# Performance work log

Measured on AMD Instinct MI355X. Metric: run time of the kernel, lower is better.

The kernel has to match this reference:

```python
import jax, jax.numpy as jnp
import numpy as np

B, S, D, DOUT, E = 2, 2048, 1024, 1024, 8
DH = 4 * D  # expert hidden size


def setup_inputs() -> dict:
    key = jax.random.key(0)
    ks = jax.random.split(key, 7)
    sc = lambda *sh: 1.0 / np.sqrt(sh[-2]) if len(sh) >= 2 else 0.02
    return {
        "x": jax.random.normal(ks[0], (B, S, D), jnp.float32),
        "Wg": jax.random.normal(ks[1], (D, E), jnp.float32) / np.sqrt(D),
        "bg": jnp.zeros((E,), jnp.float32),
        "W1": jax.random.normal(ks[2], (E, D, DH), jnp.float32) / np.sqrt(D),
        "b1": jax.random.normal(ks[3], (E, DH), jnp.float32) * 0.02,
        "W2": jax.random.normal(ks[4], (E, DH, DOUT), jnp.float32) / np.sqrt(DH),
        "b2": jax.random.normal(ks[5], (E, DOUT), jnp.float32) * 0.02,
    }


def reference(x, Wg, bg, W1, b1, W2, b2):
    # x: [B, S, D] -> flatten tokens (chunking over seq in the original is
    # math-neutral: routing and expert MLP are per-token).
    Bb, Ss, Dd = x.shape
    xt = x.reshape(-1, Dd)                       # [T, D]
    # Gate: softmax then argmax (top-1 routing, output NOT scaled by gate prob)
    gates = jax.nn.softmax(xt @ Wg + bg, axis=-1)  # [T, E]
    sel = jnp.argmax(gates, axis=-1)               # [T]
    nE = W1.shape[0]
    out = jnp.zeros((xt.shape[0], W2.shape[-1]), x.dtype)
    # Grouped expert MLP expressed as masked dense loop over the small fixed
    # expert count (jit-friendly; a fused gather-grouped-GEMM-scatter kernel
    # is the optimization target).
    for e in range(nE):
        h = jax.nn.gelu(xt @ W1[e] + b1[e], approximate=False)  # [T, 4D]
        ye = h @ W2[e] + b2[e]                                  # [T, DOUT]
        out = jnp.where((sel == e)[:, None], ye, out)
    return out.reshape(Bb, Ss, -1)
```

## Files before the change

kernel.cpp:

```cpp
#include <hip/hip_runtime.h>
#include <hip/hip_bf16.h>
#include <math.h>

#define T_TOK 4096
#define DIM   1024
#define NEXP  8
#define DHID  4096
#define NDOUT 1024
#define BM    128
#define MAXTILES 40

typedef short bf16x8 __attribute__((ext_vector_type(8)));
typedef float f32x4 __attribute__((ext_vector_type(4)));

__device__ __forceinline__ unsigned short f2bf(float f) {
  unsigned u = __float_as_uint(f);
  u += 0x7fffu + ((u >> 16) & 1u);
  return (unsigned short)(u >> 16);
}
__device__ __forceinline__ unsigned pack2bf(float a, float b) {
  return (unsigned)f2bf(a) | ((unsigned)f2bf(b) << 16);
}
__device__ __forceinline__ void gl_lds16(const void* g, void* l) {
  __builtin_amdgcn_global_load_lds(
      (const __attribute__((address_space(1))) void*)g,
      (__attribute__((address_space(3))) void*)l, 16, 0, 0);
}

__global__ __launch_bounds__(256)
void gate_kernel(const float* __restrict__ x, const float* __restrict__ Wg,
                 const float* __restrict__ bg, int* __restrict__ sel) {
  int lane = threadIdx.x & 63;
  int wid  = threadIdx.x >> 6;
  int t = blockIdx.x * 4 + wid;
  if (t >= T_TOK) return;
  const float* xr = x + (size_t)t * DIM;
  double acc[NEXP];
#pragma unroll
  for (int e = 0; e < NEXP; e++) acc[e] = 0.0;
  for (int j = 0; j < DIM / 64; j++) {
    int d = lane + j * 64;
    float xv = xr[d];
    const float4* wr = reinterpret_cast<const float4*>(Wg + (size_t)d * NEXP);
    float4 w0 = wr[0], w1 = wr[1];
    acc[0] += (double)xv * (double)w0.x;
    acc[1] += (double)xv * (double)w0.y;
    acc[2] += (double)xv * (double)w0.z;
    acc[3] += (double)xv * (double)w0.w;
    acc[4] += (double)xv * (double)w1.x;
    acc[5] += (double)xv * (double)w1.y;
    acc[6] += (double)xv * (double)w1.z;
    acc[7] += (double)xv * (double)w1.w;
  }
#pragma unroll
  for (int off = 32; off >= 1; off >>= 1) {
#pragma unroll
    for (int e = 0; e < NEXP; e++) acc[e] += __shfl_down(acc[e], off);
  }
  if (lane == 0) {
    double best = acc[0] + (double)bg[0];
    int bi = 0;
#pragma unroll
    for (int e = 1; e < NEXP; e++) {
      double v = acc[e] + (double)bg[e];
      if (v > best) { best = v; bi = e; }
    }
    sel[t] = bi;
  }
}

__global__ void zero_kernel(int* __restrict__ counts) {
  if (threadIdx.x < NEXP) counts[threadIdx.x] = 0;
}

__global__ void hist_kernel(const int* __restrict__ sel, int* __restrict__ counts) {
  __shared__ int lc[NEXP];
  if (threadIdx.x < NEXP) lc[threadIdx.x] = 0;
  __syncthreads();
  int t = blockIdx.x * 256 + threadIdx.x;
  atomicAdd(&lc[sel[t]], 1);
  __syncthreads();
  if (threadIdx.x < NEXP) atomicAdd(&counts[threadIdx.x], lc[threadIdx.x]);
}

__global__ void plan_kernel(const int* __restrict__ counts, int* __restrict__ base,
                            int* __restrict__ cursor, int* __restrict__ tileExpert,
                            int* __restrict__ tilePos, int* __restrict__ tileRows,
                            int* __restrict__ ntiles) {
  if (threadIdx.x == 0) {
    int acc = 0, nt = 0;
    for (int e = 0; e < NEXP; e++) {
      base[e] = acc; cursor[e] = acc;
      int c = counts[e];
      for (int j = 0; j < c; j += BM) {
        tileExpert[nt] = e;
        tilePos[nt]    = acc + j;
        int rem = c - j;
        tileRows[nt]   = rem < BM ? rem : BM;
        nt++;
      }
      acc += c;
    }
    *ntiles = nt;
  }
}

__global__ void scatter_kernel(const int* __restrict__ sel, int* __restrict__ cursor,
                               int* __restrict__ list) {
  __shared__ int lcnt[NEXP];
  __shared__ int lbase[NEXP];
  int tid = threadIdx.x;
  if (tid < NEXP) lcnt[tid] = 0;
  __syncthreads();
  int t = blockIdx.x * 256 + tid;
  int e = sel[t];
  int lpos = atomicAdd(&lcnt[e], 1);
  __syncthreads();
  if (tid < NEXP) lbase[tid] = atomicAdd(&cursor[tid], lcnt[tid]);
  __syncthreads();
  list[lbase[e] + lpos] = t;
}

__global__ __launch_bounds__(256)
void convert_x_kernel(const float* __restrict__ x, unsigned short* __restrict__ xbf) {
  int i = (blockIdx.x * 256 + threadIdx.x) * 8;
  float4 a = *(const float4*)(x + i);
  float4 b = *(const float4*)(x + i + 4);
  uint4 o;
  o.x = pack2bf(a.x, a.y); o.y = pack2bf(a.z, a.w);
  o.z = pack2bf(b.x, b.y); o.w = pack2bf(b.z, b.w);
  *(uint4*)(xbf + i) = o;
}

__global__ __launch_bounds__(256)
void transpose_convert_kernel(const float* __restrict__ in, unsigned short* __restrict__ out,
                              int K, int N) {
  int nb = blockIdx.x, kb = blockIdx.y, e = blockIdx.z;
  const float* inp = in + (size_t)e * K * N;
  unsigned short* outp = out + (size_t)e * N * K;
  __shared__ unsigned short lds[64][72];
  int tx = threadIdx.x;
  int kloc = tx >> 4;
  int n4   = (tx & 15) << 2;
#pragma unroll
  for (int p = 0; p < 4; p++) {
    int k = p * 16 + kloc;
    float4 v = *(const float4*)(inp + (size_t)(kb * 64 + k) * N + nb * 64 + n4);
    lds[n4 + 0][k] = f2bf(v.x);
    lds[n4 + 1][k] = f2bf(v.y);
    lds[n4 + 2][k] = f2bf(v.z);
    lds[n4 + 3][k] = f2bf(v.w);
  }
  __syncthreads();
  int n  = tx >> 2;
  int kq = (tx & 3) << 4;
  uint4 a = *(const uint4*)&lds[n][kq];
  uint4 b = *(const uint4*)&lds[n][kq + 8];
  unsigned short* o = outp + (size_t)(nb * 64 + n) * K + kb * 64 + kq;
  *(uint4*)o = a;
  *(uint4*)(o + 8) = b;
}


__global__ __launch_bounds__(256)
void gemm1_kernel(const unsigned short* __restrict__ xbf, const unsigned short* __restrict__ W1T,
                  const float* __restrict__ b1, const int* __restrict__ list,
                  const int* __restrict__ tileExpert, const int* __restrict__ tilePos,
                  const int* __restrict__ tileRows, const int* __restrict__ ntiles,
                  unsigned short* __restrict__ Hc) {
  int tIdx = blockIdx.y;
  if (tIdx >= *ntiles) return;
  int e = tileExpert[tIdx], posBase = tilePos[tIdx], rows = tileRows[tIdx];
  int n0 = blockIdx.x * 128;

  __shared__ __align__(1024) char As[128 * 128];
  __shared__ __align__(1024) char Bs[128 * 128];

  const int tx = threadIdx.x, lane = tx & 63, w = tx >> 6;
  const int wm = w >> 1, wn = w & 1;
  const int rsub = lane >> 3;
  const int px = ((lane & 7) ^ rsub) << 4;

  const char* aS[4];
  const char* bS[4];
#pragma unroll
  for (int j = 0; j < 4; j++) {
    int r = w * 32 + j * 8 + rsub;
    int tok = list[posBase + (r < rows ? r : rows - 1)];
    aS[j] = (const char*)xbf + (size_t)tok * (DIM * 2) + px;
    bS[j] = (const char*)W1T + ((size_t)e * DHID + n0 + r) * (DIM * 2) + px;
  }

  f32x4 acc[4][4];
#pragma unroll
  for (int mf = 0; mf < 4; mf++)
#pragma unroll
    for (int nf = 0; nf < 4; nf++)
      acc[mf][nf] = f32x4{0.f, 0.f, 0.f, 0.f};

  const int NT = DIM / 64;
  for (int kt = 0; kt < NT; kt++) {
    int kb = kt * 128;
#pragma unroll
    for (int j = 0; j < 4; j++) {
      gl_lds16(aS[j] + kb, &As[(w * 32 + j * 8) * 128]);
      gl_lds16(bS[j] + kb, &Bs[(w * 32 + j * 8) * 128]);
    }
    __syncthreads();
#pragma unroll
    for (int ks = 0; ks < 2; ks++) {
      int koff = (ks * 64 + (lane >> 4) * 16) ^ ((lane & 7) << 4);
      bf16x8 aF[4], bF[4];
#pragma unroll
      for (int mf = 0; mf < 4; mf++)
        aF[mf] = *(const bf16x8*)&As[(wm * 64 + mf * 16 + (lane & 15)) * 128 + koff];
#pragma unroll
      for (int nf = 0; nf < 4; nf++)
        bF[nf] = *(const bf16x8*)&Bs[(wn * 64 + nf * 16 + (lane & 15)) * 128 + koff];
#pragma unroll
      for (int mf = 0; mf < 4; mf++)
#pragma unroll
        for (int nf = 0; nf < 4; nf++)
          acc[mf][nf] = __builtin_amdgcn_mfma_f32_16x16x32_bf16(aF[mf], bF[nf], acc[mf][nf], 0, 0, 0);
    }
    __syncthreads();
  }

  const float* b1e = b1 + (size_t)e * DHID;
#pragma unroll
  for (int nf = 0; nf < 4; nf++) {
    int col = n0 + wn * 64 + nf * 16 + (lane & 15);
    float bias = b1e[col];
#pragma unroll
    for (int mf = 0; mf < 4; mf++) {
#pragma unroll
      for (int j = 0; j < 4; j++) {
        int rloc = wm * 64 + mf * 16 + ((lane >> 4) << 2) + j;
        if (rloc < rows) {
          float h = acc[mf][nf][j] + bias;
          float g = 0.5f * h * (1.0f + erff(h * 0.70710678118654752f));
          Hc[(size_t)(posBase + rloc) * DHID + col] = f2bf(g);
        }
      }
    }
  }
}

__global__ __launch_bounds__(256)
void gemm2_kernel(const unsigned short* __restrict__ Hc, const unsigned short* __restrict__ W2T,
                  const float* __restrict__ b2, const int* __restrict__ tileExpert,
                  const int* __restrict__ tilePos, const int* __restrict__ tileRows,
                  const int* __restrict__ ntiles, float* __restrict__ Ppart) {
  int tIdx = blockIdx.y;
  if (tIdx >= *ntiles) return;
  int e = tileExpert[tIdx], posBase = tilePos[tIdx], rows = tileRows[tIdx];
  int n0 = blockIdx.x * 128;
  int zs = blockIdx.z;
  size_t kbyte0 = (size_t)zs * 32 * 128;

  __shared__ __align__(1024) char As[128 * 128];
  __shared__ __align__(1024) char Bs[128 * 128];

  const int tx = threadIdx.x, lane = tx & 63, w = tx >> 6;
  const int wm = w >> 1, wn = w & 1;
  const int rsub = lane >> 3;
  const int px = ((lane & 7) ^ rsub) << 4;

  const char* aS[4];
  const char* bS[4];
#pragma unroll
  for (int j = 0; j < 4; j++) {
    int r = w * 32 + j * 8 + rsub;
    int ar = posBase + (r < rows ? r : rows - 1);
    aS[j] = (const char*)Hc + (size_t)ar * (DHID * 2) + kbyte0 + px;
    bS[j] = (const char*)W2T + ((size_t)e * NDOUT + n0 + r) * (DHID * 2) + kbyte0 + px;
  }

  f32x4 acc[4][4];
#pragma unroll
  for (int mf = 0; mf < 4; mf++)
#pragma unroll
    for (int nf = 0; nf < 4; nf++)
      acc[mf][nf] = f32x4{0.f, 0.f, 0.f, 0.f};

  const int NT = 32;
  for (int kt = 0; kt < NT; kt++) {
    int kb = kt * 128;
#pragma unroll
    for (int j = 0; j < 4; j++) {
      gl_lds16(aS[j] + kb, &As[(w * 32 + j * 8) * 128]);
      gl_lds16(bS[j] + kb, &Bs[(w * 32 + j * 8) * 128]);
    }
    __syncthreads();
#pragma unroll
    for (int ks = 0; ks < 2; ks++) {
      int koff = (ks * 64 + (lane >> 4) * 16) ^ ((lane & 7) << 4);
      bf16x8 aF[4], bF[4];
#pragma unroll
      for (int mf = 0; mf < 4; mf++)
        aF[mf] = *(const bf16x8*)&As[(wm * 64 + mf * 16 + (lane & 15)) * 128 + koff];
#pragma unroll
      for (int nf = 0; nf < 4; nf++)
        bF[nf] = *(const bf16x8*)&Bs[(wn * 64 + nf * 16 + (lane & 15)) * 128 + koff];
#pragma unroll
      for (int mf = 0; mf < 4; mf++)
#pragma unroll
        for (int nf = 0; nf < 4; nf++)
          acc[mf][nf] = __builtin_amdgcn_mfma_f32_16x16x32_bf16(aF[mf], bF[nf], acc[mf][nf], 0, 0, 0);
    }
    __syncthreads();
  }

  const float* b2e = b2 + (size_t)e * NDOUT;
  float* P = Ppart + (size_t)zs * T_TOK * NDOUT;
#pragma unroll
  for (int nf = 0; nf < 4; nf++) {
    int col = n0 + wn * 64 + nf * 16 + (lane & 15);
    float bias = (zs == 0) ? b2e[col] : 0.f;
#pragma unroll
    for (int mf = 0; mf < 4; mf++)
#pragma unroll
      for (int j = 0; j < 4; j++) {
        int rloc = wm * 64 + mf * 16 + ((lane >> 4) << 2) + j;
        if (rloc < rows)
          P[(size_t)(posBase + rloc) * NDOUT + col] = acc[mf][nf][j] + bias;
      }
  }
}

__global__ __launch_bounds__(256)
void reduce_kernel(const float* __restrict__ Ppart, const int* __restrict__ list,
                   float* __restrict__ out) {
  int pos = blockIdx.x;
  int tok = list[pos];
  int c = threadIdx.x * 4;
  float4 a = *(const float4*)(Ppart + (size_t)pos * NDOUT + c);
  float4 b = *(const float4*)(Ppart + (size_t)T_TOK * NDOUT + (size_t)pos * NDOUT + c);
  float4 o; o.x = a.x + b.x; o.y = a.y + b.y; o.z = a.z + b.z; o.w = a.w + b.w;
  *(float4*)(out + (size_t)tok * NDOUT + c) = o;
}

extern "C" void kernel_launch(void* const* d_in, const int* in_sizes, int n_in,
                              void* d_out, int out_size, void* d_ws, size_t ws_size,
                              hipStream_t stream) {
  const float* x  = (const float*)d_in[0];
  const float* Wg = (const float*)d_in[1];
  const float* bg = (const float*)d_in[2];
  const float* W1 = (const float*)d_in[3];
  const float* b1 = (const float*)d_in[4];
  const float* W2 = (const float*)d_in[5];
  const float* b2 = (const float*)d_in[6];
  float* out = (float*)d_out;

  char* ws = (char*)d_ws;
  int* sel        = (int*)(ws);
  int* counts     = (int*)(ws + 16384);
  int* base       = (int*)(ws + 16448);
  int* cursor     = (int*)(ws + 16512);
  int* ntiles     = (int*)(ws + 16576);
  int* tileExpert = (int*)(ws + 16640);
  int* tilePos    = (int*)(ws + 16832);
  int* tileRows   = (int*)(ws + 17024);
  int* list       = (int*)(ws + 17408);

  unsigned short* xbf = (unsigned short*)(ws + (1ull << 20));
  unsigned short* Hc  = (unsigned short*)(ws + (16ull << 20));
  unsigned short* W1T = (unsigned short*)(ws + (48ull << 20));
  unsigned short* W2T = (unsigned short*)(ws + (112ull << 20));
  float* Ppart        = (float*)(ws + (48ull << 20));

  gate_kernel<<<T_TOK / 4, 256, 0, stream>>>(x, Wg, bg, sel);
  zero_kernel<<<1, 64, 0, stream>>>(counts);
  hist_kernel<<<T_TOK / 256, 256, 0, stream>>>(sel, counts);
  plan_kernel<<<1, 64, 0, stream>>>(counts, base, cursor, tileExpert, tilePos, tileRows, ntiles);
  scatter_kernel<<<T_TOK / 256, 256, 0, stream>>>(sel, cursor, list);

  convert_x_kernel<<<T_TOK * DIM / (256 * 8), 256, 0, stream>>>(x, xbf);
  transpose_convert_kernel<<<dim3(DHID / 64, DIM / 64, NEXP), 256, 0, stream>>>(W1, W1T, DIM, DHID);
  transpose_convert_kernel<<<dim3(NDOUT / 64, DHID / 64, NEXP), 256, 0, stream>>>(W2, W2T, DHID, NDOUT);

  gemm1_kernel<<<dim3(DHID / 128, MAXTILES), 256, 0, stream>>>(
      xbf, W1T, b1, list, tileExpert, tilePos, tileRows, ntiles, Hc);
  gemm2_kernel<<<dim3(NDOUT / 128, MAXTILES, 2), 256, 0, stream>>>(
      Hc, W2T, b2, tileExpert, tilePos, tileRows, ntiles, Ppart);
  reduce_kernel<<<T_TOK, 256, 0, stream>>>(Ppart, list, out);
}
```

Baseline: 328.2 us.

## Store weights and hidden activations in pre-swizzled contiguous tile layout

The transpose kernel now writes W1/W2 as contiguous 128x64 bf16 tiles with the LDS XOR swizzle already applied. gemm1 writes its GELU output into the same per-tile swizzled layout. gemm2 and gemm1 can then fill LDS from fully contiguous 16 KB chunks instead of strided row gathers. The goal is better global-load coalescing and simpler address math. The cost is that gemm1's stores become scattered 2-byte writes, padded rows are written unconditionally, and the workspace offsets are reshuffled.

```diff
diff --git a/kernel.cpp b/kernel.cpp
--- a/kernel.cpp
+++ b/kernel.cpp
@@ -133,32 +133,33 @@
 }
 
 __global__ __launch_bounds__(256)
-void transpose_convert_kernel(const float* __restrict__ in, unsigned short* __restrict__ out,
-                              int K, int N) {
+void transpose_tile_kernel(const float* __restrict__ in, unsigned short* __restrict__ out,
+                           int K, int N) {
   int nb = blockIdx.x, kb = blockIdx.y, e = blockIdx.z;
   const float* inp = in + (size_t)e * K * N;
-  unsigned short* outp = out + (size_t)e * N * K;
-  __shared__ unsigned short lds[64][72];
+  __shared__ unsigned short lds[128][72];
   int tx = threadIdx.x;
-  int kloc = tx >> 4;
-  int n4   = (tx & 15) << 2;
-#pragma unroll
-  for (int p = 0; p < 4; p++) {
-    int k = p * 16 + kloc;
-    float4 v = *(const float4*)(inp + (size_t)(kb * 64 + k) * N + nb * 64 + n4);
+  int kloc = tx >> 5;
+  int n4   = (tx & 31) << 2;
+#pragma unroll
+  for (int p = 0; p < 8; p++) {
+    int k = p * 8 + kloc;
+    float4 v = *(const float4*)(inp + (size_t)(kb * 64 + k) * N + nb * 128 + n4);
     lds[n4 + 0][k] = f2bf(v.x);
     lds[n4 + 1][k] = f2bf(v.y);
     lds[n4 + 2][k] = f2bf(v.z);
     lds[n4 + 3][k] = f2bf(v.w);
   }
   __syncthreads();
-  int n  = tx >> 2;
-  int kq = (tx & 3) << 4;
-  uint4 a = *(const uint4*)&lds[n][kq];
-  uint4 b = *(const uint4*)&lds[n][kq + 8];
-  unsigned short* o = outp + (size_t)(nb * 64 + n) * K + kb * 64 + kq;
-  *(uint4*)o = a;
-  *(uint4*)(o + 8) = b;
+  char* tile = (char*)(out + (((size_t)e * gridDim.x + nb) * gridDim.y + kb) * 8192);
+  int r  = tx >> 1;
+  int kc0 = (tx & 1) * 32;
+#pragma unroll
+  for (int c = 0; c < 4; c++) {
+    int kc = kc0 + c * 8;
+    uint4 v = *(const uint4*)&lds[r][kc];
+    *(uint4*)(tile + r * 128 + ((2 * kc) ^ ((r & 7) << 4))) = v;
+  }
 }
 
 
@@ -167,11 +168,11 @@
                   const float* __restrict__ b1, const int* __restrict__ list,
                   const int* __restrict__ tileExpert, const int* __restrict__ tilePos,
                   const int* __restrict__ tileRows, const int* __restrict__ ntiles,
-                  unsigned short* __restrict__ Hc) {
+                  unsigned short* __restrict__ HcT) {
   int tIdx = blockIdx.y;
   if (tIdx >= *ntiles) return;
   int e = tileExpert[tIdx], posBase = tilePos[tIdx], rows = tileRows[tIdx];
-  int n0 = blockIdx.x * 128;
+  int nb = blockIdx.x;
 
   __shared__ __align__(1024) char As[128 * 128];
   __shared__ __align__(1024) char Bs[128 * 128];
@@ -182,14 +183,14 @@
   const int px = ((lane & 7) ^ rsub) << 4;
 
   const char* aS[4];
-  const char* bS[4];
 #pragma unroll
   for (int j = 0; j < 4; j++) {
     int r = w * 32 + j * 8 + rsub;
     int tok = list[posBase + (r < rows ? r : rows - 1)];
     aS[j] = (const char*)xbf + (size_t)tok * (DIM * 2) + px;
-    bS[j] = (const char*)W1T + ((size_t)e * DHID + n0 + r) * (DIM * 2) + px;
-  }
+  }
+  const char* bTile = (const char*)W1T + (((size_t)e * (DHID / 128) + nb) * (DIM / 64)) * 16384
+                      + w * 4096 + lane * 16;
 
   f32x4 acc[4][4];
 #pragma unroll
@@ -200,11 +201,10 @@
 
   const int NT = DIM / 64;
   for (int kt = 0; kt < NT; kt++) {
-    int kb = kt * 128;
 #pragma unroll
     for (int j = 0; j < 4; j++) {
-      gl_lds16(aS[j] + kb, &As[(w * 32 + j * 8) * 128]);
-      gl_lds16(bS[j] + kb, &Bs[(w * 32 + j * 8) * 128]);
+      gl_lds16(aS[j] + kt * 128, &As[(w * 32 + j * 8) * 128]);
+      gl_lds16(bTile + kt * 16384 + j * 1024, &Bs[w * 4096 + j * 1024]);
     }
     __syncthreads();
 #pragma unroll
@@ -227,54 +227,48 @@
   }
 
   const float* b1e = b1 + (size_t)e * DHID;
+  char* hBase = (char*)(HcT + (size_t)tIdx * (DHID / 64) * 8192);
 #pragma unroll
   for (int nf = 0; nf < 4; nf++) {
-    int col = n0 + wn * 64 + nf * 16 + (lane & 15);
+    int col = nb * 128 + wn * 64 + nf * 16 + (lane & 15);
+    int kt2 = col >> 6;
+    int colk2 = (col & 63) * 2;
     float bias = b1e[col];
+    char* tile = hBase + (size_t)kt2 * 16384;
 #pragma unroll
     for (int mf = 0; mf < 4; mf++) {
 #pragma unroll
       for (int j = 0; j < 4; j++) {
-        int rloc = wm * 64 + mf * 16 + ((lane >> 4) << 2) + j;
-        if (rloc < rows) {
-          float h = acc[mf][nf][j] + bias;
-          float g = 0.5f * h * (1.0f + erff(h * 0.70710678118654752f));
-          Hc[(size_t)(posBase + rloc) * DHID + col] = f2bf(g);
-        }
+        int r = wm * 64 + mf * 16 + ((lane >> 4) << 2) + j;
+        float h = acc[mf][nf][j] + bias;
+        float g = 0.5f * h * (1.0f + erff(h * 0.70710678118654752f));
+        *(unsigned short*)(tile + r * 128 + (colk2 ^ ((r & 7) << 4))) = f2bf(g);
       }
     }
   }
 }
 
 __global__ __launch_bounds__(256)
-void gemm2_kernel(const unsigned short* __restrict__ Hc, const unsigned short* __restrict__ W2T,
+void gemm2_kernel(const unsigned short* __restrict__ HcT, const unsigned short* __restrict__ W2T,
                   const float* __restrict__ b2, const int* __restrict__ tileExpert,
                   const int* __restrict__ tilePos, const int* __restrict__ tileRows,
                   const int* __restrict__ ntiles, float* __restrict__ Ppart) {
   int tIdx = blockIdx.y;
   if (tIdx >= *ntiles) return;
   int e = tileExpert[tIdx], posBase = tilePos[tIdx], rows = tileRows[tIdx];
-  int n0 = blockIdx.x * 128;
+  int nb = blockIdx.x;
   int zs = blockIdx.z;
-  size_t kbyte0 = (size_t)zs * 32 * 128;
 
   __shared__ __align__(1024) char As[128 * 128];
   __shared__ __align__(1024) char Bs[128 * 128];
 
   const int tx = threadIdx.x, lane = tx & 63, w = tx >> 6;
   const int wm = w >> 1, wn = w & 1;
-  const int rsub = lane >> 3;
-  const int px = ((lane & 7) ^ rsub) << 4;
-
-  const char* aS[4];
-  const char* bS[4];
-#pragma unroll
-  for (int j = 0; j < 4; j++) {
-    int r = w * 32 + j * 8 + rsub;
-    int ar = posBase + (r < rows ? r : rows - 1);
-    aS[j] = (const char*)Hc + (size_t)ar * (DHID * 2) + kbyte0 + px;
-    bS[j] = (const char*)W2T + ((size_t)e * NDOUT + n0 + r) * (DHID * 2) + kbyte0 + px;
-  }
+
+  const char* aTile = (const char*)HcT + (size_t)tIdx * (DHID / 64) * 16384
+                      + (size_t)zs * 32 * 16384 + w * 4096 + lane * 16;
+  const char* bTile = (const char*)W2T + (((size_t)e * (NDOUT / 128) + nb) * (DHID / 64)) * 16384
+                      + (size_t)zs * 32 * 16384 + w * 4096 + lane * 16;
 
   f32x4 acc[4][4];
 #pragma unroll
@@ -285,11 +279,10 @@
 
   const int NT = 32;
   for (int kt = 0; kt < NT; kt++) {
-    int kb = kt * 128;
 #pragma unroll
     for (int j = 0; j < 4; j++) {
-      gl_lds16(aS[j] + kb, &As[(w * 32 + j * 8) * 128]);
-      gl_lds16(bS[j] + kb, &Bs[(w * 32 + j * 8) * 128]);
+      gl_lds16(aTile + kt * 16384 + j * 1024, &As[w * 4096 + j * 1024]);
+      gl_lds16(bTile + kt * 16384 + j * 1024, &Bs[w * 4096 + j * 1024]);
     }
     __syncthreads();
 #pragma unroll
@@ -315,7 +308,7 @@
   float* P = Ppart + (size_t)zs * T_TOK * NDOUT;
 #pragma unroll
   for (int nf = 0; nf < 4; nf++) {
-    int col = n0 + wn * 64 + nf * 16 + (lane & 15);
+    int col = nb * 128 + wn * 64 + nf * 16 + (lane & 15);
     float bias = (zs == 0) ? b2e[col] : 0.f;
 #pragma unroll
     for (int mf = 0; mf < 4; mf++)
@@ -364,10 +357,10 @@
   int* list       = (int*)(ws + 17408);
 
   unsigned short* xbf = (unsigned short*)(ws + (1ull << 20));
-  unsigned short* Hc  = (unsigned short*)(ws + (16ull << 20));
-  unsigned short* W1T = (unsigned short*)(ws + (48ull << 20));
-  unsigned short* W2T = (unsigned short*)(ws + (112ull << 20));
-  float* Ppart        = (float*)(ws + (48ull << 20));
+  unsigned short* HcT = (unsigned short*)(ws + (10ull << 20));
+  unsigned short* W1T = (unsigned short*)(ws + (52ull << 20));
+  unsigned short* W2T = (unsigned short*)(ws + (116ull << 20));
+  float* Ppart        = (float*)(ws + (52ull << 20));
 
   gate_kernel<<<T_TOK / 4, 256, 0, stream>>>(x, Wg, bg, sel);
   zero_kernel<<<1, 64, 0, stream>>>(counts);
@@ -376,12 +369,12 @@
   scatter_kernel<<<T_TOK / 256, 256, 0, stream>>>(sel, cursor, list);
 
   convert_x_kernel<<<T_TOK * DIM / (256 * 8), 256, 0, stream>>>(x, xbf);
-  transpose_convert_kernel<<<dim3(DHID / 64, DIM / 64, NEXP), 256, 0, stream>>>(W1, W1T, DIM, DHID);
-  transpose_convert_kernel<<<dim3(NDOUT / 64, DHID / 64, NEXP), 256, 0, stream>>>(W2, W2T, DHID, NDOUT);
+  transpose_tile_kernel<<<dim3(DHID / 128, DIM / 64, NEXP), 256, 0, stream>>>(W1, W1T, DIM, DHID);
+  transpose_tile_kernel<<<dim3(NDOUT / 128, DHID / 64, NEXP), 256, 0, stream>>>(W2, W2T, DHID, NDOUT);
 
   gemm1_kernel<<<dim3(DHID / 128, MAXTILES), 256, 0, stream>>>(
-      xbf, W1T, b1, list, tileExpert, tilePos, tileRows, ntiles, Hc);
+      xbf, W1T, b1, list, tileExpert, tilePos, tileRows, ntiles, HcT);
   gemm2_kernel<<<dim3(NDOUT / 128, MAXTILES, 2), 256, 0, stream>>>(
-      Hc, W2T, b2, tileExpert, tilePos, tileRows, ntiles, Ppart);
+      HcT, W2T, b2, tileExpert, tilePos, tileRows, ntiles, Ppart);
   reduce_kernel<<<T_TOK, 256, 0, stream>>>(Ppart, list, out);
 }
```

After: 307.5 us. 1.07x faster.
